# Kernel optimization log

Measured on AMD Instinct MI355X. Metric: run time of the kernel, lower is better.

Reference implementation:

```python
import jax, jax.numpy as jnp
import numpy as np

N, E, R, D = 50000, 640000, 200, 128  # nodes, edges, relations, feat dim (in_feat==out_feat)
EPS = 1e-5  # LayerNorm eps
NEG_SLOPE = 0.01  # F.leaky_relu default

def _xavier(k, shape):
    gain = np.sqrt(2.0)  # calculate_gain('relu')
    std = gain * np.sqrt(2.0 / (shape[0] + shape[1]))
    a = np.sqrt(3.0) * std
    return jax.random.uniform(k, shape, jnp.float32, -a, a)

def setup_inputs() -> dict:
    key = jax.random.key(0)
    ks = jax.random.split(key, 10)
    return {
        "node": jax.random.normal(ks[0], (N, D), jnp.float32),
        "rel": jax.random.normal(ks[1], (R, D), jnp.float32),
        "norm": jax.random.uniform(ks[2], (N, 1), jnp.float32),
        "w_triplet": _xavier(ks[3], (3 * D, D)),
        "w_quad": _xavier(ks[4], (D, D)),
        "loop_weight": _xavier(ks[5], (D, D)),
        "evolve_loop_weight": _xavier(ks[6], (D, D)),
        "src": jax.random.randint(ks[7], (E,), 0, N),
        "dst": jax.random.randint(ks[8], (E,), 0, N),
        "etype": jax.random.randint(ks[9], (E,), 0, R),
    }

def reference(node, rel, norm, w_triplet, w_quad, loop_weight, evolve_loop_weight, src, dst, etype):
    # triplet = cat([h_src, rel_emb, h_dst], 1) @ w_triplet, computed blockwise
    # to avoid materializing the [E, 3D] concat.
    W_s, W_r, W_d = w_triplet[:D], w_triplet[D:2 * D], w_triplet[2 * D:]
    triplet = node[src] @ W_s + rel[etype] @ W_r + node[dst] @ W_d  # [E, D]
    # 'fre' not in edata -> sro_fre is zeros; a_triplet = triplet @ w_quad
    a = jax.nn.leaky_relu(triplet @ w_quad, negative_slope=NEG_SLOPE)  # [E, D]
    # edge_softmax: softmax over incoming edges per destination node, per feature
    a_max = jax.ops.segment_max(a, dst, num_segments=N)
    a_max = jnp.where(jnp.isfinite(a_max), a_max, 0.0)  # empty segments -> -inf
    ex = jnp.exp(a - a_max[dst])
    denom = jax.ops.segment_sum(ex, dst, num_segments=N)
    att = ex / denom[dst]
    # weighted scatter-sum aggregation, then apply_func: h * norm
    h = jax.ops.segment_sum(att * triplet, dst, num_segments=N) * norm  # [N, D]
    # self-loop: evolve_loop_weight for in-degree-0 nodes, loop_weight otherwise
    indeg = jax.ops.segment_sum(jnp.ones((E,), jnp.float32), dst, num_segments=N)
    loop = jnp.where((indeg > 0)[:, None], node @ loop_weight, node @ evolve_loop_weight)
    out = h + loop
    # LayerNorm(elementwise_affine=False)
    mu = jnp.mean(out, axis=-1, keepdims=True)
    var = jnp.var(out, axis=-1, keepdims=True)
    return (out - mu) * jax.lax.rsqrt(var + EPS)
```

## Files before the change

kernel.cpp:

```cpp
#include <hip/hip_runtime.h>
#include <hip/hip_bf16.h>

#define D 128
#define LOG2E 1.4426950408889634f

typedef __attribute__((ext_vector_type(8))) short bf16x8;
typedef __attribute__((ext_vector_type(4))) float f32x4;

__device__ __forceinline__ unsigned short f2bf_bits(float f) {
    union { __hip_bfloat16 h; unsigned short u; } c;
    c.h = __float2bfloat16(f);
    return c.u;
}
__device__ __forceinline__ float bfbits2f(unsigned short u) {
    return __uint_as_float(((unsigned)u) << 16);
}
__device__ __forceinline__ float ldf(const void* p, size_t i, int f32) {
    return f32 ? ((const float*)p)[i] : bfbits2f(((const unsigned short*)p)[i]);
}
__device__ __forceinline__ void unpk(unsigned u, float& a, float& b) {
    a = __uint_as_float(u << 16);
    b = __uint_as_float(u & 0xFFFF0000u);
}

__global__ __launch_bounds__(256) void prep_kernel(
    const void* __restrict__ node, const void* __restrict__ wtrip,
    const void* __restrict__ wquad, const void* __restrict__ loopW,
    const void* __restrict__ evoW, unsigned short* __restrict__ wT,
    int* __restrict__ cnt, int* __restrict__ rank,
    const int* __restrict__ dst, int* __restrict__ flag, int E) {
    __shared__ int sflag;
    int tid = threadIdx.x;
    int bad = 0;
    if (tid < 64) {
        for (int j = 0; j < 4; j++) {
            float v = bfbits2f(((const unsigned short*)node)[tid + 64 * j]);
            if (!(fabsf(v) < 1e4f)) bad = 1;
        }
    }
    unsigned long long m = __ballot(bad);
    if (tid == 0) sflag = (m != 0ull) ? 1 : 0;
    __syncthreads();
    int f32 = sflag;
    int bx = blockIdx.x;
    if (bx == 0 && tid == 0) *flag = f32;

    if (bx < 192) {
        int unit = bx * 2 + (tid >> 7);
        int k = unit & 127, mjob = unit >> 7;
        int t = tid & 127;
        float acc = 0.f;
        for (int j = 0; j < D; j++)
            acc += ldf(wtrip, (size_t)mjob * D * D + (size_t)k * D + j, f32) *
                   ldf(wquad, (size_t)j * D + t, f32);
        const int jmap0 = (mjob == 0) ? 0 : (mjob == 1 ? 6 : 2);
        wT[(size_t)jmap0 * D * D + (size_t)t * D + k] = f2bf_bits(acc);
    } else if (bx < 272) {
        int u = bx - 192;
        int jr = u >> 4, seg = u & 15;
        const void* srcp; size_t base; int j;
        switch (jr) {
            case 0: srcp = wtrip; base = 0;             j = 1; break;
            case 1: srcp = wtrip; base = 2 * D * D;     j = 3; break;
            case 2: srcp = loopW; base = 0;             j = 4; break;
            case 3: srcp = evoW;  base = 0;             j = 5; break;
            default: srcp = wtrip; base = (size_t)D * D; j = 7; break;
        }
        for (int c = tid; c < 1024; c += 256) {
            int idx = seg * 1024 + c;
            int n = idx >> 7, k = idx & 127;
            unsigned short b = f32 ? f2bf_bits(((const float*)srcp)[base + (size_t)k * D + n])
                                   : ((const unsigned short*)srcp)[base + (size_t)k * D + n];
            wT[(size_t)j * D * D + (size_t)n * D + k] = b;
        }
    } else {
        int e = (bx - 272) * 256 + tid;
        if (e < E) rank[e] = atomicAdd(&cnt[dst[e]], 1);
    }
}

__global__ void scan_block(const int* __restrict__ cnt, int* __restrict__ offs,
                           int* __restrict__ part, int N) {
    __shared__ int sh[256];
    int tid = threadIdx.x;
    int i = blockIdx.x * 256 + tid;
    int v = (i < N) ? cnt[i] : 0;
    sh[tid] = v;
    __syncthreads();
    for (int o = 1; o < 256; o <<= 1) {
        int t = (tid >= o) ? sh[tid - o] : 0;
        __syncthreads();
        sh[tid] += t;
        __syncthreads();
    }
    if (i < N) offs[i] = sh[tid] - v;
    if (tid == 255) part[blockIdx.x] = sh[255];
}

__global__ void scan_fix(int* __restrict__ offs, const int* __restrict__ part,
                         int N, int E) {
    __shared__ int sh[256];
    int tid = threadIdx.x, b = blockIdx.x;
    sh[tid] = (tid < b) ? part[tid] : 0;
    __syncthreads();
    for (int o = 128; o; o >>= 1) {
        if (tid < o) sh[tid] += sh[tid + o];
        __syncthreads();
    }
    int carry = sh[0];
    int i = b * 256 + tid;
    if (i < N) offs[i] += carry;
    if (b == 0 && tid == 0) offs[N] = E;
}

__global__ __launch_bounds__(512) void gemm_kernel(
    const void* __restrict__ node, const void* __restrict__ rel,
    const unsigned short* __restrict__ wT, const int* __restrict__ cnt,
    unsigned* __restrict__ nodeST, unsigned* __restrict__ nodeDT,
    unsigned* __restrict__ relRT, unsigned* __restrict__ loopSel,
    const int* __restrict__ flag, int N, int R, int nodeBlocks,
    const int* __restrict__ src, const int* __restrict__ dst,
    const int* __restrict__ et, const int* __restrict__ offs,
    const int* __restrict__ rank, unsigned* __restrict__ ePack, int E) {
    __shared__ __align__(16) unsigned short Wt[D][D + 8];

    int bx = blockIdx.x, by = blockIdx.y;
    int tid = threadIdx.y * 64 + threadIdx.x;
    int isRel = 0, jp;
    if (bx >= nodeBlocks) {
        if (by == 1) {
            int e = (bx - nodeBlocks) * 512 + tid;
            if (e < E) {
                int d = dst[e];
                ePack[offs[d] + rank[e]] = (unsigned)src[e] | ((unsigned)et[e] << 20);
            }
            return;
        }
        if (by != 0 || bx - nodeBlocks >= (R + 127) / 128) return;
        isRel = 1;
        jp = 3;
    } else {
        jp = by;
    }

    int f32 = *flag;
    int rows = isRel ? R : N;
    int row0 = (isRel ? bx - nodeBlocks : bx) * 128;
    const void* A = isRel ? rel : node;

    int lane = threadIdx.x, wv = threadIdx.y;
    int l16 = lane & 15, quad = lane >> 4;
    int ar = row0 + wv * 16 + l16;
    int ar_c = ar < rows ? ar : rows - 1;

    int qIdx, tIdx;
    unsigned* O = nullptr;
    switch (jp) {
        case 0: qIdx = 0; tIdx = 1; O = nodeST; break;
        case 1: qIdx = 2; tIdx = 3; O = nodeDT; break;
        case 2: qIdx = 4; tIdx = 5; break;
        default: qIdx = 6; tIdx = 7; O = relRT; break;
    }

    bf16x8 af[4];
#pragma unroll
    for (int kk = 0; kk < 4; kk++) {
        int k = kk * 32 + quad * 8;
        if (f32) {
            const float* Af = (const float*)A + (size_t)ar_c * D + k;
#pragma unroll
            for (int j = 0; j < 8; j++) af[kk][j] = (short)f2bf_bits(Af[j]);
        } else {
            af[kk] = *(const bf16x8*)((const unsigned short*)A + (size_t)ar_c * D + k);
        }
    }

    const unsigned short* gQ = wT + (size_t)qIdx * D * D;
    const unsigned short* gT = wT + (size_t)tIdx * D * D;

    bf16x8 wreg[4], wreg2[4];
#pragma unroll
    for (int i = 0; i < 4; i++) {
        int c = tid + i * 512;
        wreg[i] = *(const bf16x8*)(gQ + (c >> 4) * 128 + (c & 15) * 8);
    }

    f32x4 accQ[8], accT[8];
#pragma unroll
    for (int i = 0; i < 8; i++) {
        accQ[i] = (f32x4){0.f, 0.f, 0.f, 0.f};
        accT[i] = (f32x4){0.f, 0.f, 0.f, 0.f};
    }

    for (int pass = 0; pass < 2; pass++) {
#pragma unroll
        for (int i = 0; i < 4; i++) {
            int c = tid + i * 512;
            *(bf16x8*)(&Wt[c >> 4][(c & 15) * 8]) = wreg[i];
        }
        if (pass == 0) {
#pragma unroll
            for (int i = 0; i < 4; i++) {
                int c = tid + i * 512;
                wreg2[i] = *(const bf16x8*)(gT + (c >> 4) * 128 + (c & 15) * 8);
            }
        }
        __syncthreads();
        f32x4* acc = pass ? accT : accQ;
#pragma unroll
        for (int kk = 0; kk < 4; kk++) {
#pragma unroll
            for (int nt = 0; nt < 8; nt++) {
                bf16x8 bfr = *(const bf16x8*)(&Wt[nt * 16 + l16][kk * 32 + quad * 8]);
                acc[nt] = __builtin_amdgcn_mfma_f32_16x16x32_bf16(af[kk], bfr, acc[nt], 0, 0, 0);
            }
        }
        __syncthreads();
#pragma unroll
        for (int i = 0; i < 4; i++) wreg[i] = wreg2[i];
    }

    int cr0 = row0 + wv * 16 + quad * 4;
    int odd = l16 & 1;
    if (jp != 2) {
#pragma unroll
        for (int r = 0; r < 4; r++) {
            int cr = cr0 + r;
#pragma unroll
            for (int nt = 0; nt < 8; nt++) {
                float vQ = accQ[nt][r] * LOG2E;
                float vT = accT[nt][r];
                float oQ = __shfl_xor(vQ, 1);
                float oT = __shfl_xor(vT, 1);
                unsigned w;
                if (!odd) w = (unsigned)f2bf_bits(vQ) | ((unsigned)f2bf_bits(oQ) << 16);
                else      w = (unsigned)f2bf_bits(oT) | ((unsigned)f2bf_bits(vT) << 16);
                if (cr < rows) O[(size_t)cr * 128 + nt * 16 + l16] = w;
            }
        }
    } else {
#pragma unroll
        for (int r = 0; r < 4; r++) {
            int cr = cr0 + r;
            int deg = (cr < rows) ? cnt[cr] : 0;
#pragma unroll
            for (int nt = 0; nt < 8; nt++) {
                float vL = accQ[nt][r], vE = accT[nt][r];
                float oL = __shfl_xor(vL, 1);
                float oE = __shfl_xor(vE, 1);
                unsigned wl, we;
                if (!odd) {
                    wl = (unsigned)f2bf_bits(vL) | ((unsigned)f2bf_bits(oL) << 16);
                    we = (unsigned)f2bf_bits(vE) | ((unsigned)f2bf_bits(oE) << 16);
                } else {
                    wl = (unsigned)f2bf_bits(oL) | ((unsigned)f2bf_bits(vL) << 16);
                    we = (unsigned)f2bf_bits(oE) | ((unsigned)f2bf_bits(vE) << 16);
                }
                if (cr < rows && !odd)
                    loopSel[(size_t)cr * 64 + nt * 8 + (l16 >> 1)] = (deg > 0) ? wl : we;
            }
        }
    }
}

__global__ __launch_bounds__(256) void agg_kernel(
    const int* __restrict__ offs, const unsigned* __restrict__ ePack,
    const uint2* __restrict__ ST, const uint2* __restrict__ RT,
    const uint2* __restrict__ DT, const unsigned* __restrict__ loopSel,
    const void* __restrict__ normv, void* __restrict__ out,
    const int* __restrict__ flag, int N) {
    int n = blockIdx.x * 4 + threadIdx.y;
    if (n >= N) return;
    int f32 = *flag;
    int lane = threadIdx.x;
    int start = offs[n], end = offs[n + 1];
    int deg = end - start;

    unsigned ul = loopSel[(size_t)n * 64 + lane];
    uint2 ud = DT[(size_t)n * 64 + lane];
    float qd0, qd1, td0, td1, acc0, acc1;
    unpk(ud.x, qd0, qd1);
    unpk(ud.y, td0, td1);
    unpk(ul, acc0, acc1);

    float den0 = 0.f, den1 = 0.f, h0 = 0.f, h1 = 0.f;
#define GATH(PK, US, UR)                                              \
    uint2 US = ST[(size_t)((PK) & 0xFFFFFu) * 64 + lane];             \
    uint2 UR = RT[(size_t)((PK) >> 20) * 64 + lane];
#define EMATH(US, UR)                                                 \
    {                                                                 \
        float qs0, qs1, qr0, qr1, ts0, ts1, tr0, tr1;                 \
        unpk(US.x, qs0, qs1); unpk(UR.x, qr0, qr1);                   \
        unpk(US.y, ts0, ts1); unpk(UR.y, tr0, tr1);                   \
        float q0 = qs0 + qr0 + qd0, q1 = qs1 + qr1 + qd1;             \
        float a0 = q0 > 0.f ? q0 : 0.01f * q0;                        \
        float a1 = q1 > 0.f ? q1 : 0.01f * q1;                        \
        float ex0 = exp2f(a0), ex1 = exp2f(a1);                       \
        den0 += ex0; den1 += ex1;                                     \
        h0 += ex0 * (ts0 + tr0 + td0);                                \
        h1 += ex1 * (ts1 + tr1 + td1);                                \
    }
    int e = start;
    for (; e + 3 < end; e += 4) {
        unsigned p0 = ePack[e], p1 = ePack[e + 1], p2 = ePack[e + 2], p3 = ePack[e + 3];
        GATH(p0, sA, rA)
        GATH(p1, sB, rB)
        GATH(p2, sC, rC)
        GATH(p3, sD, rD)
        EMATH(sA, rA)
        EMATH(sB, rB)
        EMATH(sC, rC)
        EMATH(sD, rD)
    }
    for (; e < end; e++) {
        unsigned pp = ePack[e];
        GATH(pp, sE, rE)
        EMATH(sE, rE)
    }

    float x0, x1;
    if (deg > 0) {
        float nrm = ldf(normv, n, f32);
        x0 = h0 / den0 * nrm + acc0;
        x1 = h1 / den1 * nrm + acc1;
    } else {
        x0 = acc0;
        x1 = acc1;
    }

    float s = x0 + x1, ss = x0 * x0 + x1 * x1;
#pragma unroll
    for (int o = 32; o; o >>= 1) {
        s += __shfl_xor(s, o);
        ss += __shfl_xor(ss, o);
    }
    float mu = s * (1.f / 128.f);
    float var = ss * (1.f / 128.f) - mu * mu;
    float rstd = rsqrtf(var + 1e-5f);
    float y0 = (x0 - mu) * rstd, y1 = (x1 - mu) * rstd;

    if (f32) {
        ((float2*)out)[(size_t)n * 64 + lane] = make_float2(y0, y1);
    } else {
        unsigned ob = (unsigned)f2bf_bits(y0) | ((unsigned)f2bf_bits(y1) << 16);
        ((unsigned*)out)[(size_t)n * 64 + lane] = ob;
    }
}

extern "C" void kernel_launch(void* const* d_in, const int* in_sizes, int n_in,
                              void* d_out, int out_size, void* d_ws, size_t ws_size,
                              hipStream_t stream) {
    const void* node = d_in[0];
    const void* rel = d_in[1];
    const void* normv = d_in[2];
    const void* wtrip = d_in[3];
    const void* wquad = d_in[4];
    const void* loopW = d_in[5];
    const void* evoW = d_in[6];
    const int* src = (const int*)d_in[7];
    const int* dst = (const int*)d_in[8];
    const int* et = (const int*)d_in[9];

    int N = in_sizes[0] / D;
    int R = in_sizes[1] / D;
    int E = in_sizes[7];
    int nb = (N + 255) / 256;
    int nodeBlocks = (N + 127) / 128;
    int relBlocks = (R + 127) / 128;
    int scatBlocks = (E + 511) / 512;

    char* p = (char*)d_ws;
    auto alloc = [&](size_t bytes) -> void* {
        void* r = (void*)p;
        p += (bytes + 255) & ~(size_t)255;
        return r;
    };
    unsigned* nodeST = (unsigned*)alloc((size_t)N * 128 * 4);
    unsigned* nodeDT = (unsigned*)alloc((size_t)N * 128 * 4);
    unsigned* relRT = (unsigned*)alloc((size_t)R * 128 * 4);
    unsigned* loopSel = (unsigned*)alloc((size_t)N * 64 * 4);
    unsigned short* wT = (unsigned short*)alloc((size_t)8 * D * D * 2);
    int* cnt = (int*)alloc((size_t)N * 4);
    int* offs = (int*)alloc((size_t)(N + 1) * 4);
    int* part = (int*)alloc((size_t)(nb + 1) * 4);
    int* rank = (int*)alloc((size_t)E * 4);
    unsigned* ePack = (unsigned*)alloc((size_t)E * 4);
    int* flag = (int*)alloc(4);

    hipMemsetAsync(cnt, 0, (size_t)N * 4, stream);
    prep_kernel<<<272 + (E + 255) / 256, 256, 0, stream>>>(
        node, wtrip, wquad, loopW, evoW, wT, cnt, rank, dst, flag, E);
    scan_block<<<nb, 256, 0, stream>>>(cnt, offs, part, N);
    scan_fix<<<nb, 256, 0, stream>>>(offs, part, N, E);
    int xext = nodeBlocks + (scatBlocks > relBlocks ? scatBlocks : relBlocks);
    gemm_kernel<<<dim3(xext, 3), dim3(64, 8), 0, stream>>>(
        node, rel, wT, cnt, nodeST, nodeDT, relRT, loopSel, flag, N, R, nodeBlocks,
        src, dst, et, offs, rank, ePack, E);
    agg_kernel<<<(N + 3) / 4, dim3(64, 4), 0, stream>>>(
        offs, ePack, (const uint2*)nodeST, (const uint2*)relRT, (const uint2*)nodeDT,
        loopSel, normv, d_out, flag, N);
}
```

Measured before the change: 236.1 us.

## Merge scan kernels and streamline aggregation loop with masked tail and hoisted dst term

Replaces the two-kernel block scan plus fixup with a single kernel in which each block recomputes its carry by summing all preceding counts directly, removing one launch and the partials buffer at the cost of redundant reads of cnt. In the aggregation kernel, the destination-feature term is moved out of the per-edge weighted sum, since softmax weights sum to one. The scalar tail loop becomes one masked four-wide batch so its gathers can overlap. It also uses 32-bit index arithmetic, fmaxf for leaky relu, and sets an occupancy hint in launch bounds.

```diff
diff --git a/kernel.cpp b/kernel.cpp
--- a/kernel.cpp
+++ b/kernel.cpp
@@ -79,11 +79,12 @@
     }
 }
 
-__global__ void scan_block(const int* __restrict__ cnt, int* __restrict__ offs,
-                           int* __restrict__ part, int N) {
+__global__ void scan_kernel(const int* __restrict__ cnt, int* __restrict__ offs,
+                            int N, int E) {
     __shared__ int sh[256];
-    int tid = threadIdx.x;
-    int i = blockIdx.x * 256 + tid;
+    int tid = threadIdx.x, b = blockIdx.x;
+    int base = b * 256;
+    int i = base + tid;
     int v = (i < N) ? cnt[i] : 0;
     sh[tid] = v;
     __syncthreads();
@@ -93,23 +94,18 @@
         sh[tid] += t;
         __syncthreads();
     }
-    if (i < N) offs[i] = sh[tid] - v;
-    if (tid == 255) part[blockIdx.x] = sh[255];
-}
-
-__global__ void scan_fix(int* __restrict__ offs, const int* __restrict__ part,
-                         int N, int E) {
-    __shared__ int sh[256];
-    int tid = threadIdx.x, b = blockIdx.x;
-    sh[tid] = (tid < b) ? part[tid] : 0;
+    int local = sh[tid] - v;
+    __syncthreads();
+    int part = 0;
+    for (int j = tid; j < base; j += 256) part += cnt[j];
+    sh[tid] = part;
     __syncthreads();
     for (int o = 128; o; o >>= 1) {
         if (tid < o) sh[tid] += sh[tid + o];
         __syncthreads();
     }
     int carry = sh[0];
-    int i = b * 256 + tid;
-    if (i < N) offs[i] += carry;
+    if (i < N) offs[i] = local + carry;
     if (b == 0 && tid == 0) offs[N] = E;
 }
 
@@ -263,7 +259,7 @@
     }
 }
 
-__global__ __launch_bounds__(256) void agg_kernel(
+__global__ __launch_bounds__(256, 4) void agg_kernel(
     const int* __restrict__ offs, const unsigned* __restrict__ ePack,
     const uint2* __restrict__ ST, const uint2* __restrict__ RT,
     const uint2* __restrict__ DT, const unsigned* __restrict__ loopSel,
@@ -276,53 +272,59 @@
     int start = offs[n], end = offs[n + 1];
     int deg = end - start;
 
-    unsigned ul = loopSel[(size_t)n * 64 + lane];
-    uint2 ud = DT[(size_t)n * 64 + lane];
+    unsigned ul = loopSel[(unsigned)n * 64u + lane];
+    uint2 ud = DT[(unsigned)n * 64u + lane];
     float qd0, qd1, td0, td1, acc0, acc1;
     unpk(ud.x, qd0, qd1);
     unpk(ud.y, td0, td1);
     unpk(ul, acc0, acc1);
 
     float den0 = 0.f, den1 = 0.f, h0 = 0.f, h1 = 0.f;
-#define GATH(PK, US, UR)                                              \
-    uint2 US = ST[(size_t)((PK) & 0xFFFFFu) * 64 + lane];             \
-    uint2 UR = RT[(size_t)((PK) >> 20) * 64 + lane];
-#define EMATH(US, UR)                                                 \
+#define EMATH(US, UR, MSK)                                            \
     {                                                                 \
         float qs0, qs1, qr0, qr1, ts0, ts1, tr0, tr1;                 \
         unpk(US.x, qs0, qs1); unpk(UR.x, qr0, qr1);                   \
         unpk(US.y, ts0, ts1); unpk(UR.y, tr0, tr1);                   \
         float q0 = qs0 + qr0 + qd0, q1 = qs1 + qr1 + qd1;             \
-        float a0 = q0 > 0.f ? q0 : 0.01f * q0;                        \
-        float a1 = q1 > 0.f ? q1 : 0.01f * q1;                        \
-        float ex0 = exp2f(a0), ex1 = exp2f(a1);                       \
+        float a0 = fmaxf(q0, 0.01f * q0);                             \
+        float a1 = fmaxf(q1, 0.01f * q1);                             \
+        float ex0 = exp2f(a0) * (MSK), ex1 = exp2f(a1) * (MSK);       \
         den0 += ex0; den1 += ex1;                                     \
-        h0 += ex0 * (ts0 + tr0 + td0);                                \
-        h1 += ex1 * (ts1 + tr1 + td1);                                \
+        h0 += ex0 * (ts0 + tr0);                                      \
+        h1 += ex1 * (ts1 + tr1);                                      \
     }
     int e = start;
     for (; e + 3 < end; e += 4) {
-        unsigned p0 = ePack[e], p1 = ePack[e + 1], p2 = ePack[e + 2], p3 = ePack[e + 3];
-        GATH(p0, sA, rA)
-        GATH(p1, sB, rB)
-        GATH(p2, sC, rC)
-        GATH(p3, sD, rD)
-        EMATH(sA, rA)
-        EMATH(sB, rB)
-        EMATH(sC, rC)
-        EMATH(sD, rD)
-    }
-    for (; e < end; e++) {
-        unsigned pp = ePack[e];
-        GATH(pp, sE, rE)
-        EMATH(sE, rE)
+        uint2 us[4], ur[4];
+#pragma unroll
+        for (int j = 0; j < 4; j++) {
+            unsigned pk = ePack[e + j];
+            us[j] = ST[((pk & 0xFFFFFu) << 6) | (unsigned)lane];
+            ur[j] = RT[((pk >> 20) << 6) | (unsigned)lane];
+        }
+#pragma unroll
+        for (int j = 0; j < 4; j++) EMATH(us[j], ur[j], 1.0f)
+    }
+    if (e < end) {
+        uint2 us[4], ur[4];
+        float mk[4];
+#pragma unroll
+        for (int j = 0; j < 4; j++) {
+            int ej = e + j < end ? e + j : end - 1;
+            mk[j] = (e + j < end) ? 1.0f : 0.0f;
+            unsigned pk = ePack[ej];
+            us[j] = ST[((pk & 0xFFFFFu) << 6) | (unsigned)lane];
+            ur[j] = RT[((pk >> 20) << 6) | (unsigned)lane];
+        }
+#pragma unroll
+        for (int j = 0; j < 4; j++) EMATH(us[j], ur[j], mk[j])
     }
 
     float x0, x1;
     if (deg > 0) {
         float nrm = ldf(normv, n, f32);
-        x0 = h0 / den0 * nrm + acc0;
-        x1 = h1 / den1 * nrm + acc1;
+        x0 = (h0 / den0 + td0) * nrm + acc0;
+        x1 = (h1 / den1 + td1) * nrm + acc1;
     } else {
         x0 = acc0;
         x1 = acc1;
@@ -340,10 +342,10 @@
     float y0 = (x0 - mu) * rstd, y1 = (x1 - mu) * rstd;
 
     if (f32) {
-        ((float2*)out)[(size_t)n * 64 + lane] = make_float2(y0, y1);
+        ((float2*)out)[(unsigned)n * 64u + lane] = make_float2(y0, y1);
     } else {
         unsigned ob = (unsigned)f2bf_bits(y0) | ((unsigned)f2bf_bits(y1) << 16);
-        ((unsigned*)out)[(size_t)n * 64 + lane] = ob;
+        ((unsigned*)out)[(unsigned)n * 64u + lane] = ob;
     }
 }
 
@@ -382,7 +384,6 @@
     unsigned short* wT = (unsigned short*)alloc((size_t)8 * D * D * 2);
     int* cnt = (int*)alloc((size_t)N * 4);
     int* offs = (int*)alloc((size_t)(N + 1) * 4);
-    int* part = (int*)alloc((size_t)(nb + 1) * 4);
     int* rank = (int*)alloc((size_t)E * 4);
     unsigned* ePack = (unsigned*)alloc((size_t)E * 4);
     int* flag = (int*)alloc(4);
@@ -390,8 +391,7 @@
     hipMemsetAsync(cnt, 0, (size_t)N * 4, stream);
     prep_kernel<<<272 + (E + 255) / 256, 256, 0, stream>>>(
         node, wtrip, wquad, loopW, evoW, wT, cnt, rank, dst, flag, E);
-    scan_block<<<nb, 256, 0, stream>>>(cnt, offs, part, N);
-    scan_fix<<<nb, 256, 0, stream>>>(offs, part, N, E);
+    scan_kernel<<<nb, 256, 0, stream>>>(cnt, offs, N, E);
     int xext = nodeBlocks + (scatBlocks > relBlocks ? scatBlocks : relBlocks);
     gemm_kernel<<<dim3(xext, 3), dim3(64, 8), 0, stream>>>(
         node, rel, wT, cnt, nodeST, nodeDT, relRT, loopSel, flag, N, R, nodeBlocks,
```

Result: slower. 258.0 us (+9.3%).
